# Kernel optimization log

Hardware: AMD Instinct MI355X
Metric: run time of the kernel (lower is better)

The kernel has to match this reference:

```python
import jax, jax.numpy as jnp
import numpy as np

FDIM = 512
MAX_LEN = 200
B = 16
K_CELLS = 1024
EPS = 1e-5


def setup_inputs() -> dict:
    key = jax.random.key(0)
    ks = jax.random.split(key, 16)
    s = 0.02
    return {
        "src": jax.random.normal(ks[0], (B, MAX_LEN, 33), jnp.float32),
        "prom": jax.random.normal(ks[1], (B, 32), jnp.float32),
        "atac": jax.random.uniform(ks[2], (B, K_CELLS, MAX_LEN), jnp.float32),
        "mask": jax.random.uniform(ks[3], (B, MAX_LEN), jnp.float32),
        # prom_q: Linear(32, 32*fdim)
        "Wq_p": jax.random.normal(ks[4], (32 * FDIM, 32), jnp.float32) * s,
        "bq_p": jax.random.normal(ks[5], (32 * FDIM,), jnp.float32) * s,
        # enha_q: Linear(33, 32*fdim)
        "Wq_e": jax.random.normal(ks[6], (32 * FDIM, 33), jnp.float32) * s,
        "bq_e": jax.random.normal(ks[7], (32 * FDIM,), jnp.float32) * s,
        # prom_sig: Linear(32, 1)
        "Wsig": jax.random.normal(ks[8], (1, 32), jnp.float32) * s,
        "bsig": jax.random.normal(ks[9], (1,), jnp.float32) * s,
        # encoder: Linear(fdim,128) -> ReLU -> Dropout(eval) -> Linear(128,64)
        "W1": jax.random.normal(ks[10], (128, FDIM), jnp.float32) * s,
        "b1": jax.random.normal(ks[11], (128,), jnp.float32) * s,
        "W2": jax.random.normal(ks[12], (64, 128), jnp.float32) * s,
        "b2": jax.random.normal(ks[13], (64,), jnp.float32) * s,
    }


def reference(src, prom, atac, mask, Wq_p, bq_p, Wq_e, bq_e, Wsig, bsig, W1, b1, W2, b2):
    b = prom.shape[0]
    # prom_qm: [B, fdim, 32]
    prom_qm = (prom @ Wq_p.T + bq_p).reshape(b, FDIM, 32)
    # enha_km: [B, max_len, 32, fdim]
    enha_km = (src @ Wq_e.T + bq_e).reshape(b, MAX_LEN, 32, FDIM)
    # QK = prom_qm[b,f,1,32] @ enha_km.transpose(1,3)[b,f,32,L] -> [B, fdim, L]
    QK = jnp.einsum("bfk,blkf->bfl", prom_qm, enha_km)
    # mask multiply (broadcast over fdim)
    QK = QK * mask[:, None, :]
    # slice off promoter column, LayerNorm over last dim, no affine
    QKs = QK[:, :, 1:MAX_LEN]  # [B, fdim, L-1]
    mu = jnp.mean(QKs, axis=-1, keepdims=True)
    var = jnp.var(QKs, axis=-1, keepdims=True)
    QKs = (QKs - mu) * jax.lax.rsqrt(var + EPS)
    # prom_sig: [B, fdim, 1]
    prom_qms = jnp.einsum("bfk,k->bf", prom_qm, Wsig[0]) + bsig[0]
    # atac: [B, K, L] -> transpose -> [B, L, K]
    atac_t = jnp.swapaxes(atac, 1, 2)
    atac_s = atac_t[:, 1:MAX_LEN, :]  # [B, L-1, K]
    atac_p = atac_t[:, 0, :]          # [B, K]
    # aggregation: [B, fdim, K]
    QKall = jnp.einsum("bfl,blk->bfk", QKs, atac_s) + prom_qms[:, :, None] * atac_p[:, None, :]
    # [B, K, fdim]
    QKall = jnp.swapaxes(QKall, 1, 2)
    # encoder MLP (dropout inactive at eval)
    h = jax.nn.relu(QKall @ W1.T + b1)
    out = h @ W2.T + b2  # [B, K, 64]
    return out
```

## Files before the change

kernel.cpp:

```cpp
#include <hip/hip_runtime.h>

#define B_ 16
#define FDIM_ 512
#define LMAX_ 200
#define KC_ 1024
#define KPAD_ 256

typedef __attribute__((ext_vector_type(8)))  _Float16 f16x8;
typedef __attribute__((ext_vector_type(4)))  float    floatx4;

__global__ __launch_bounds__(256) void k_prep(
    const float* __restrict__ prom, const float* __restrict__ Wq_p,
    const float* __restrict__ bq_p, const float* __restrict__ Wq_e,
    const float* __restrict__ bq_e, const float* __restrict__ Wsig,
    const float* __restrict__ bsig,
    float* __restrict__ Aout, float* __restrict__ Cout, float* __restrict__ Pout)
{
    int f = blockIdx.x;
    int tid = threadIdx.x;

    __shared__ float Wp[32][33];
    __shared__ float We[32][33];
    __shared__ float promS[16][32];
    __shared__ float pqS[16][33];
    __shared__ float bqpS[32], bqeS[32], wsigS[32];

    for (int i = tid; i < 1024; i += 256)
        Wp[i >> 5][i & 31] = Wq_p[(size_t)f * 1024 + i];
    if (tid < 128) ((float4*)&promS[0][0])[tid] = ((const float4*)prom)[tid];
    for (int i = tid; i < 32 * 33; i += 256) {
        int k = i / 33, j = i - k * 33;
        We[k][j] = Wq_e[((size_t)(k * 512 + f)) * 33 + j];
    }
    if (tid < 32) {
        bqpS[tid]  = bq_p[f * 32 + tid];
        bqeS[tid]  = bq_e[tid * 512 + f];
        wsigS[tid] = Wsig[tid];
    }
    __syncthreads();

    for (int i = tid; i < 512; i += 256) {
        int b = i >> 5, k = i & 31;
        float s = bqpS[k];
        #pragma unroll
        for (int j = 0; j < 32; ++j) s += promS[b][j] * Wp[k][j];
        pqS[b][k] = s;
    }
    __syncthreads();

    for (int i = tid; i < 16 * 33; i += 256) {
        int b = i / 33, j = i - b * 33;
        float s = 0.f;
        #pragma unroll
        for (int k = 0; k < 32; ++k) s += pqS[b][k] * We[k][j];
        Aout[((size_t)(b * 512 + f)) * 33 + j] = s;
    }
    if (tid < 16) {
        int b = tid;
        float c = 0.f, p = bsig[0];
        #pragma unroll
        for (int k = 0; k < 32; ++k) {
            c += pqS[b][k] * bqeS[k];
            p += pqS[b][k] * wsigS[k];
        }
        Cout[b * 512 + f] = c;
        Pout[b * 512 + f] = p;
    }
}

__global__ __launch_bounds__(256) void k_qk_ln(
    const float* __restrict__ src, const float* __restrict__ mask,
    const float* __restrict__ A, const float* __restrict__ C,
    const float* __restrict__ P, _Float16* __restrict__ SB)
{
    __shared__ float srcF[6600];
    __shared__ float maskS[200];

    int tid = threadIdx.x;
    int b = blockIdx.x >> 6;
    int fc = blockIdx.x & 63;
    int f_sub = tid >> 5, l_loc = tid & 31;
    int f = fc * 8 + f_sub;
    int wid = b * 512 + f;

    for (int i = tid; i < 6600; i += 256) srcF[i] = src[(size_t)b * 6600 + i];
    for (int i = tid; i < 200; i += 256)  maskS[i] = mask[b * 200 + i];

    float Ar[33];
    const float* Ap = A + (size_t)wid * 33;
    #pragma unroll
    for (int j = 0; j < 33; ++j) Ar[j] = Ap[j];
    float Cv = C[wid], Pv = P[wid];
    __syncthreads();

    float vals[8];
    float s1 = 0.f, s2 = 0.f;
    #pragma unroll
    for (int t = 0; t < 8; ++t) {
        int l = l_loc + 32 * t;
        float v = 0.f;
        if (l < LMAX_) {
            const float* sp = &srcF[l * 33];
            float s = Cv;
            #pragma unroll
            for (int j = 0; j < 33; ++j) s += sp[j] * Ar[j];
            v = s * maskS[l];
            if (l >= 1) { s1 += v; s2 += v * v; }
        }
        vals[t] = v;
    }
    #pragma unroll
    for (int off = 16; off > 0; off >>= 1) {
        s1 += __shfl_xor(s1, off, 64);
        s2 += __shfl_xor(s2, off, 64);
    }
    float mu  = s1 * (1.f / 199.f);
    float var = s2 * (1.f / 199.f) - mu * mu;
    float inv = 1.0f / sqrtf(var + 1e-5f);

    _Float16* Sp = SB + (size_t)wid * KPAD_;
    #pragma unroll
    for (int t = 0; t < 8; ++t) {
        int l = l_loc + 32 * t;
        float v = (l == 0) ? Pv : ((l < LMAX_) ? (vals[t] - mu) * inv : 0.f);
        Sp[l] = (_Float16)v;
    }
}

__global__ __launch_bounds__(256) void k_fused(
    const float* __restrict__ atac, const _Float16* __restrict__ SB,
    const float* __restrict__ W1, const float* __restrict__ b1,
    const float* __restrict__ W2, const float* __restrict__ b2,
    float* __restrict__ out)
{
    __shared__ _Float16 lds[61440];
    _Float16* At  = lds;
    _Float16* Wt  = lds + 4096;
    _Float16* W2t = lds + 12288;
    _Float16* Ht  = lds + 20480;
    _Float16* Bt  = lds + 28672;
    _Float16* Qt  = Bt;

    int tid = threadIdx.x, lane = tid & 63, wid = tid >> 6;
    int l15 = lane & 15, l4 = lane >> 4;
    int b = blockIdx.x >> 4;
    int row0 = (blockIdx.x & 15) * 64;

    const float*    Ab = atac + ((size_t)b * KC_ + row0) * LMAX_;
    const _Float16* Bb = SB + (size_t)b * FDIM_ * KPAD_;

    #pragma unroll
    for (int it = 0; it < 4; ++it) {
        int i = it * 256 + tid;
        int r = i >> 4, s = i & 15;
        const float* p = W2 + r * 128 + s * 8;
        float4 v0 = *(const float4*)p;
        float4 v1 = *(const float4*)(p + 4);
        f16x8 o;
        o[0] = (_Float16)v0.x; o[1] = (_Float16)v0.y;
        o[2] = (_Float16)v0.z; o[3] = (_Float16)v0.w;
        o[4] = (_Float16)v1.x; o[5] = (_Float16)v1.y;
        o[6] = (_Float16)v1.z; o[7] = (_Float16)v1.w;
        *(f16x8*)&W2t[r * 128 + ((s ^ (r & 7)) << 3)] = o;
    }

    floatx4 acc[4][8];
    #pragma unroll
    for (int m = 0; m < 4; ++m)
        #pragma unroll
        for (int n = 0; n < 8; ++n)
            acc[m][n] = (floatx4){0.f, 0.f, 0.f, 0.f};

    for (int ch = 0; ch < 4; ++ch) {
        int k0 = ch * 64;
        #pragma unroll
        for (int it = 0; it < 2; ++it) {
            int i = it * 256 + tid;
            int r = i >> 3, s = i & 7;
            int kg = k0 + s * 8;
            f16x8 o;
            if (kg < LMAX_) {
                const float* p = Ab + (size_t)r * LMAX_ + kg;
                float4 v0 = *(const float4*)p;
                float4 v1 = *(const float4*)(p + 4);
                o[0] = (_Float16)v0.x; o[1] = (_Float16)v0.y;
                o[2] = (_Float16)v0.z; o[3] = (_Float16)v0.w;
                o[4] = (_Float16)v1.x; o[5] = (_Float16)v1.y;
                o[6] = (_Float16)v1.z; o[7] = (_Float16)v1.w;
            } else {
                #pragma unroll
                for (int j = 0; j < 8; ++j) o[j] = (_Float16)0.f;
            }
            *(f16x8*)&At[r * 64 + ((s ^ (r & 7)) << 3)] = o;
        }
        #pragma unroll
        for (int it = 0; it < 16; ++it) {
            int i = it * 256 + tid;
            int r = i >> 3, s = i & 7;
            f16x8 v = *(const f16x8*)(Bb + (size_t)r * KPAD_ + k0 + s * 8);
            *(f16x8*)&Bt[r * 64 + ((s ^ (r & 7)) << 3)] = v;
        }
        __syncthreads();
        #pragma unroll
        for (int ks = 0; ks < 2; ++ks) {
            f16x8 av[4], bv[8];
            #pragma unroll
            for (int m = 0; m < 4; ++m) {
                int row = m * 16 + l15;
                av[m] = *(const f16x8*)&At[row * 64 + (((ks * 4 + l4) ^ (row & 7)) << 3)];
            }
            #pragma unroll
            for (int n = 0; n < 8; ++n) {
                int frow = wid * 128 + n * 16 + l15;
                bv[n] = *(const f16x8*)&Bt[frow * 64 + (((ks * 4 + l4) ^ (frow & 7)) << 3)];
            }
            #pragma unroll
            for (int m = 0; m < 4; ++m)
                #pragma unroll
                for (int n = 0; n < 8; ++n)
                    acc[m][n] = __builtin_amdgcn_mfma_f32_16x16x32_f16(
                        av[m], bv[n], acc[m][n], 0, 0, 0);
        }
        __syncthreads();
    }

    #pragma unroll
    for (int m = 0; m < 4; ++m) {
        #pragma unroll
        for (int n = 0; n < 8; ++n) {
            int fcol = wid * 128 + n * 16 + l15;
            int g = fcol >> 3, w = fcol & 7;
            #pragma unroll
            for (int q = 0; q < 4; ++q) {
                int row = m * 16 + l4 * 4 + q;
                Qt[row * 512 + ((g ^ (row & 7)) << 3) + w] = (_Float16)acc[m][n][q];
            }
        }
    }
    __syncthreads();

    floatx4 acc2[8];
    #pragma unroll
    for (int n = 0; n < 8; ++n) acc2[n] = (floatx4){0.f, 0.f, 0.f, 0.f};

    for (int ch = 0; ch < 8; ++ch) {
        int k0 = ch * 64;
        #pragma unroll
        for (int it = 0; it < 4; ++it) {
            int i = it * 256 + tid;
            int r = i >> 3, s = i & 7;
            const float* p = W1 + (size_t)r * 512 + k0 + s * 8;
            float4 v0 = *(const float4*)p;
            float4 v1 = *(const float4*)(p + 4);
            f16x8 o;
            o[0] = (_Float16)v0.x; o[1] = (_Float16)v0.y;
            o[2] = (_Float16)v0.z; o[3] = (_Float16)v0.w;
            o[4] = (_Float16)v1.x; o[5] = (_Float16)v1.y;
            o[6] = (_Float16)v1.z; o[7] = (_Float16)v1.w;
            *(f16x8*)&Wt[r * 64 + ((s ^ (r & 7)) << 3)] = o;
        }
        __syncthreads();
        #pragma unroll
        for (int ks = 0; ks < 2; ++ks) {
            int arow = wid * 16 + l15;
            int gk = ch * 8 + ks * 4 + l4;
            f16x8 a = *(const f16x8*)&Qt[arow * 512 + ((gk ^ (arow & 7)) << 3)];
            #pragma unroll
            for (int n = 0; n < 8; ++n) {
                int brow = n * 16 + l15;
                f16x8 bw = *(const f16x8*)&Wt[brow * 64 + (((ks * 4 + l4) ^ (brow & 7)) << 3)];
                acc2[n] = __builtin_amdgcn_mfma_f32_16x16x32_f16(a, bw, acc2[n], 0, 0, 0);
            }
        }
        __syncthreads();
    }

    #pragma unroll
    for (int n = 0; n < 8; ++n) {
        int col = n * 16 + l15;
        float bb = b1[col];
        int cg = col >> 3, cw = col & 7;
        #pragma unroll
        for (int q = 0; q < 4; ++q) {
            int row = wid * 16 + l4 * 4 + q;
            float v = fmaxf(acc2[n][q] + bb, 0.f);
            Ht[row * 128 + ((cg ^ (row & 7)) << 3) + cw] = (_Float16)v;
        }
    }
    __syncthreads();

    floatx4 acc3[4];
    #pragma unroll
    for (int n = 0; n < 4; ++n) acc3[n] = (floatx4){0.f, 0.f, 0.f, 0.f};
    #pragma unroll
    for (int ks = 0; ks < 4; ++ks) {
        int arow = wid * 16 + l15;
        f16x8 a = *(const f16x8*)&Ht[arow * 128 + (((ks * 4 + l4) ^ (arow & 7)) << 3)];
        #pragma unroll
        for (int n = 0; n < 4; ++n) {
            int brow = n * 16 + l15;
            f16x8 bw = *(const f16x8*)&W2t[brow * 128 + (((ks * 4 + l4) ^ (brow & 7)) << 3)];
            acc3[n] = __builtin_amdgcn_mfma_f32_16x16x32_f16(a, bw, acc3[n], 0, 0, 0);
        }
    }
    #pragma unroll
    for (int n = 0; n < 4; ++n) {
        float bb = b2[n * 16 + l15];
        #pragma unroll
        for (int q = 0; q < 4; ++q) {
            size_t grow = (size_t)b * KC_ + row0 + wid * 16 + l4 * 4 + q;
            out[grow * 64 + n * 16 + l15] = acc3[n][q] + bb;
        }
    }
}

extern "C" void kernel_launch(void* const* d_in, const int* in_sizes, int n_in,
                              void* d_out, int out_size, void* d_ws, size_t ws_size,
                              hipStream_t stream)
{
    const float* src  = (const float*)d_in[0];
    const float* prom = (const float*)d_in[1];
    const float* atac = (const float*)d_in[2];
    const float* mask = (const float*)d_in[3];
    const float* Wq_p = (const float*)d_in[4];
    const float* bq_p = (const float*)d_in[5];
    const float* Wq_e = (const float*)d_in[6];
    const float* bq_e = (const float*)d_in[7];
    const float* Wsig = (const float*)d_in[8];
    const float* bsig = (const float*)d_in[9];
    const float* W1   = (const float*)d_in[10];
    const float* b1   = (const float*)d_in[11];
    const float* W2   = (const float*)d_in[12];
    const float* b2   = (const float*)d_in[13];

    float* ws   = (float*)d_ws;
    float* Abuf = ws;
    float* Cbuf = Abuf + 270336;
    float* Pbuf = Cbuf + 8192;
    _Float16* SB = (_Float16*)(Pbuf + 8192);
    float* outp = (float*)d_out;

    hipLaunchKernelGGL(k_prep, dim3(512), dim3(256), 0, stream,
                       prom, Wq_p, bq_p, Wq_e, bq_e, Wsig, bsig, Abuf, Cbuf, Pbuf);

    hipLaunchKernelGGL(k_qk_ln, dim3(1024), dim3(256), 0, stream,
                       src, mask, Abuf, Cbuf, Pbuf, SB);

    hipLaunchKernelGGL(k_fused, dim3(256), dim3(256), 0, stream,
                       atac, SB, W1, b1, W2, b2, outp);
}
```

Measured before the change: 63.27 us.

## Load MFMA operands directly from global memory, drop LDS staging and barriers

The aggregation GEMM now loads atac and SB operand fragments straight from global memory into registers instead of staging them through swizzled LDS with syncthreads. The first encoder layer is re-split so each wave owns 32 output columns across all 64 rows and reads W1 fragments directly from global. W2 is read from global per fragment. LDS shrinks and launch bounds request 2 blocks per CU. This removes LDS round trips and barriers but relies on L1/L2 for reuse, uses uncoalesced per-lane row reads of atac, and raises register pressure.

```diff
diff --git a/kernel.cpp b/kernel.cpp
--- a/kernel.cpp
+++ b/kernel.cpp
@@ -8,6 +8,17 @@
 
 typedef __attribute__((ext_vector_type(8)))  _Float16 f16x8;
 typedef __attribute__((ext_vector_type(4)))  float    floatx4;
+
+__device__ __forceinline__ f16x8 ld8f(const float* __restrict__ p) {
+    float4 v0 = *(const float4*)p;
+    float4 v1 = *(const float4*)(p + 4);
+    f16x8 o;
+    o[0] = (_Float16)v0.x; o[1] = (_Float16)v0.y;
+    o[2] = (_Float16)v0.z; o[3] = (_Float16)v0.w;
+    o[4] = (_Float16)v1.x; o[5] = (_Float16)v1.y;
+    o[6] = (_Float16)v1.z; o[7] = (_Float16)v1.w;
+    return o;
+}
 
 __global__ __launch_bounds__(256) void k_prep(
     const float* __restrict__ prom, const float* __restrict__ Wq_p,
@@ -127,19 +138,15 @@
     }
 }
 
-__global__ __launch_bounds__(256) void k_fused(
+__global__ __launch_bounds__(256, 2) void k_fused(
     const float* __restrict__ atac, const _Float16* __restrict__ SB,
     const float* __restrict__ W1, const float* __restrict__ b1,
     const float* __restrict__ W2, const float* __restrict__ b2,
     float* __restrict__ out)
 {
-    __shared__ _Float16 lds[61440];
-    _Float16* At  = lds;
-    _Float16* Wt  = lds + 4096;
-    _Float16* W2t = lds + 12288;
-    _Float16* Ht  = lds + 20480;
-    _Float16* Bt  = lds + 28672;
-    _Float16* Qt  = Bt;
+    __shared__ _Float16 lds[40960];
+    _Float16* Qt = lds;
+    _Float16* Ht = lds + 32768;
 
     int tid = threadIdx.x, lane = tid & 63, wid = tid >> 6;
     int l15 = lane & 15, l4 = lane >> 4;
@@ -149,21 +156,6 @@
     const float*    Ab = atac + ((size_t)b * KC_ + row0) * LMAX_;
     const _Float16* Bb = SB + (size_t)b * FDIM_ * KPAD_;
 
-    #pragma unroll
-    for (int it = 0; it < 4; ++it) {
-        int i = it * 256 + tid;
-        int r = i >> 4, s = i & 15;
-        const float* p = W2 + r * 128 + s * 8;
-        float4 v0 = *(const float4*)p;
-        float4 v1 = *(const float4*)(p + 4);
-        f16x8 o;
-        o[0] = (_Float16)v0.x; o[1] = (_Float16)v0.y;
-        o[2] = (_Float16)v0.z; o[3] = (_Float16)v0.w;
-        o[4] = (_Float16)v1.x; o[5] = (_Float16)v1.y;
-        o[6] = (_Float16)v1.z; o[7] = (_Float16)v1.w;
-        *(f16x8*)&W2t[r * 128 + ((s ^ (r & 7)) << 3)] = o;
-    }
-
     floatx4 acc[4][8];
     #pragma unroll
     for (int m = 0; m < 4; ++m)
@@ -171,57 +163,29 @@
         for (int n = 0; n < 8; ++n)
             acc[m][n] = (floatx4){0.f, 0.f, 0.f, 0.f};
 
-    for (int ch = 0; ch < 4; ++ch) {
-        int k0 = ch * 64;
-        #pragma unroll
-        for (int it = 0; it < 2; ++it) {
-            int i = it * 256 + tid;
-            int r = i >> 3, s = i & 7;
-            int kg = k0 + s * 8;
-            f16x8 o;
-            if (kg < LMAX_) {
-                const float* p = Ab + (size_t)r * LMAX_ + kg;
-                float4 v0 = *(const float4*)p;
-                float4 v1 = *(const float4*)(p + 4);
-                o[0] = (_Float16)v0.x; o[1] = (_Float16)v0.y;
-                o[2] = (_Float16)v0.z; o[3] = (_Float16)v0.w;
-                o[4] = (_Float16)v1.x; o[5] = (_Float16)v1.y;
-                o[6] = (_Float16)v1.z; o[7] = (_Float16)v1.w;
+    #pragma unroll
+    for (int ks = 0; ks < 8; ++ks) {
+        int kg = ks * 32 + l4 * 8;
+        bool inr = kg < LMAX_;
+        f16x8 av[4], bv[8];
+        #pragma unroll
+        for (int m = 0; m < 4; ++m) {
+            if (inr) {
+                av[m] = ld8f(Ab + (size_t)(m * 16 + l15) * LMAX_ + kg);
             } else {
                 #pragma unroll
-                for (int j = 0; j < 8; ++j) o[j] = (_Float16)0.f;
+                for (int j = 0; j < 8; ++j) av[m][j] = (_Float16)0.f;
             }
-            *(f16x8*)&At[r * 64 + ((s ^ (r & 7)) << 3)] = o;
-        }
-        #pragma unroll
-        for (int it = 0; it < 16; ++it) {
-            int i = it * 256 + tid;
-            int r = i >> 3, s = i & 7;
-            f16x8 v = *(const f16x8*)(Bb + (size_t)r * KPAD_ + k0 + s * 8);
-            *(f16x8*)&Bt[r * 64 + ((s ^ (r & 7)) << 3)] = v;
-        }
-        __syncthreads();
-        #pragma unroll
-        for (int ks = 0; ks < 2; ++ks) {
-            f16x8 av[4], bv[8];
-            #pragma unroll
-            for (int m = 0; m < 4; ++m) {
-                int row = m * 16 + l15;
-                av[m] = *(const f16x8*)&At[row * 64 + (((ks * 4 + l4) ^ (row & 7)) << 3)];
-            }
-            #pragma unroll
-            for (int n = 0; n < 8; ++n) {
-                int frow = wid * 128 + n * 16 + l15;
-                bv[n] = *(const f16x8*)&Bt[frow * 64 + (((ks * 4 + l4) ^ (frow & 7)) << 3)];
-            }
-            #pragma unroll
-            for (int m = 0; m < 4; ++m)
-                #pragma unroll
-                for (int n = 0; n < 8; ++n)
-                    acc[m][n] = __builtin_amdgcn_mfma_f32_16x16x32_f16(
-                        av[m], bv[n], acc[m][n], 0, 0, 0);
-        }
-        __syncthreads();
+        }
+        #pragma unroll
+        for (int n = 0; n < 8; ++n)
+            bv[n] = *(const f16x8*)(Bb + (size_t)(wid * 128 + n * 16 + l15) * KPAD_ + kg);
+        #pragma unroll
+        for (int m = 0; m < 4; ++m)
+            #pragma unroll
+            for (int n = 0; n < 8; ++n)
+                acc[m][n] = __builtin_amdgcn_mfma_f32_16x16x32_f16(
+                    av[m], bv[n], acc[m][n], 0, 0, 0);
     }
 
     #pragma unroll
@@ -239,52 +203,46 @@
     }
     __syncthreads();
 
-    floatx4 acc2[8];
-    #pragma unroll
-    for (int n = 0; n < 8; ++n) acc2[n] = (floatx4){0.f, 0.f, 0.f, 0.f};
-
-    for (int ch = 0; ch < 8; ++ch) {
-        int k0 = ch * 64;
-        #pragma unroll
-        for (int it = 0; it < 4; ++it) {
-            int i = it * 256 + tid;
-            int r = i >> 3, s = i & 7;
-            const float* p = W1 + (size_t)r * 512 + k0 + s * 8;
-            float4 v0 = *(const float4*)p;
-            float4 v1 = *(const float4*)(p + 4);
-            f16x8 o;
-            o[0] = (_Float16)v0.x; o[1] = (_Float16)v0.y;
-            o[2] = (_Float16)v0.z; o[3] = (_Float16)v0.w;
-            o[4] = (_Float16)v1.x; o[5] = (_Float16)v1.y;
-            o[6] = (_Float16)v1.z; o[7] = (_Float16)v1.w;
-            *(f16x8*)&Wt[r * 64 + ((s ^ (r & 7)) << 3)] = o;
-        }
-        __syncthreads();
-        #pragma unroll
-        for (int ks = 0; ks < 2; ++ks) {
-            int arow = wid * 16 + l15;
-            int gk = ch * 8 + ks * 4 + l4;
-            f16x8 a = *(const f16x8*)&Qt[arow * 512 + ((gk ^ (arow & 7)) << 3)];
-            #pragma unroll
-            for (int n = 0; n < 8; ++n) {
-                int brow = n * 16 + l15;
-                f16x8 bw = *(const f16x8*)&Wt[brow * 64 + (((ks * 4 + l4) ^ (brow & 7)) << 3)];
-                acc2[n] = __builtin_amdgcn_mfma_f32_16x16x32_f16(a, bw, acc2[n], 0, 0, 0);
-            }
-        }
-        __syncthreads();
-    }
-
-    #pragma unroll
-    for (int n = 0; n < 8; ++n) {
-        int col = n * 16 + l15;
+    floatx4 acc2[4][2];
+    #pragma unroll
+    for (int m = 0; m < 4; ++m)
+        #pragma unroll
+        for (int n = 0; n < 2; ++n)
+            acc2[m][n] = (floatx4){0.f, 0.f, 0.f, 0.f};
+
+    #pragma unroll
+    for (int ks = 0; ks < 16; ++ks) {
+        int g = ks * 4 + l4;
+        f16x8 av[4], bv[2];
+        #pragma unroll
+        for (int m = 0; m < 4; ++m) {
+            int row = m * 16 + l15;
+            av[m] = *(const f16x8*)&Qt[row * 512 + ((g ^ (row & 7)) << 3)];
+        }
+        #pragma unroll
+        for (int n = 0; n < 2; ++n)
+            bv[n] = ld8f(W1 + (size_t)(wid * 32 + n * 16 + l15) * 512 + ks * 32 + l4 * 8);
+        #pragma unroll
+        for (int m = 0; m < 4; ++m)
+            #pragma unroll
+            for (int n = 0; n < 2; ++n)
+                acc2[m][n] = __builtin_amdgcn_mfma_f32_16x16x32_f16(
+                    av[m], bv[n], acc2[m][n], 0, 0, 0);
+    }
+
+    #pragma unroll
+    for (int n = 0; n < 2; ++n) {
+        int col = wid * 32 + n * 16 + l15;
         float bb = b1[col];
         int cg = col >> 3, cw = col & 7;
         #pragma unroll
-        for (int q = 0; q < 4; ++q) {
-            int row = wid * 16 + l4 * 4 + q;
-            float v = fmaxf(acc2[n][q] + bb, 0.f);
-            Ht[row * 128 + ((cg ^ (row & 7)) << 3) + cw] = (_Float16)v;
+        for (int m = 0; m < 4; ++m) {
+            #pragma unroll
+            for (int q = 0; q < 4; ++q) {
+                int row = m * 16 + l4 * 4 + q;
+                float v = fmaxf(acc2[m][n][q] + bb, 0.f);
+                Ht[row * 128 + ((cg ^ (row & 7)) << 3) + cw] = (_Float16)v;
+            }
         }
     }
     __syncthreads();
@@ -294,12 +252,12 @@
     for (int n = 0; n < 4; ++n) acc3[n] = (floatx4){0.f, 0.f, 0.f, 0.f};
     #pragma unroll
     for (int ks = 0; ks < 4; ++ks) {
+        int g = ks * 4 + l4;
         int arow = wid * 16 + l15;
-        f16x8 a = *(const f16x8*)&Ht[arow * 128 + (((ks * 4 + l4) ^ (arow & 7)) << 3)];
+        f16x8 a = *(const f16x8*)&Ht[arow * 128 + ((g ^ (arow & 7)) << 3)];
         #pragma unroll
         for (int n = 0; n < 4; ++n) {
-            int brow = n * 16 + l15;
-            f16x8 bw = *(const f16x8*)&W2t[brow * 128 + (((ks * 4 + l4) ^ (brow & 7)) << 3)];
+            f16x8 bw = ld8f(W2 + (size_t)(n * 16 + l15) * 128 + ks * 32 + l4 * 8);
             acc3[n] = __builtin_amdgcn_mfma_f32_16x16x32_f16(a, bw, acc3[n], 0, 0, 0);
         }
     }
```

Measured after the change: 58.04 us. 8.3% less time.
